# Performance work log

Measured on AMD Instinct MI355X. Metric: run time of the kernel, lower is better.

Reference implementation:

```python
import jax, jax.numpy as jnp
import numpy as np

D_MODEL = 1024
N_HEADS = 16
D_K = D_MODEL // N_HEADS
B, S = 4, 2048


def setup_inputs() -> dict:
    key = jax.random.key(0)
    ks = jax.random.split(key, 9)
    sc = 1.0 / np.sqrt(D_MODEL)
    return {
        "x": jax.random.normal(ks[0], (B, S, D_MODEL), dtype=jnp.float32),
        "Wq": jax.random.normal(ks[1], (D_MODEL, D_MODEL), dtype=jnp.float32) * sc,
        "bq": jax.random.normal(ks[2], (D_MODEL,), dtype=jnp.float32) * 0.02,
        "Wk": jax.random.normal(ks[3], (D_MODEL, D_MODEL), dtype=jnp.float32) * sc,
        "bk": jax.random.normal(ks[4], (D_MODEL,), dtype=jnp.float32) * 0.02,
        "Wv": jax.random.normal(ks[5], (D_MODEL, D_MODEL), dtype=jnp.float32) * sc,
        "bv": jax.random.normal(ks[6], (D_MODEL,), dtype=jnp.float32) * 0.02,
        "Wo": jax.random.normal(ks[7], (D_MODEL, D_MODEL), dtype=jnp.float32) * sc,
        "bo": jax.random.normal(ks[8], (D_MODEL,), dtype=jnp.float32) * 0.02,
    }


def reference(x, Wq, bq, Wk, bk, Wv, bv, Wo, bo):
    b, s, _ = x.shape
    # QKV projections (torch Linear: x @ W.T + b; here weights are stored as [in, out])
    q = (x @ Wq + bq).reshape(b, s, N_HEADS, D_K).transpose(0, 2, 1, 3)  # [b,h,s,dk]
    k = (x @ Wk + bk).reshape(b, s, N_HEADS, D_K).transpose(0, 2, 1, 3)
    v = (x @ Wv + bv).reshape(b, s, N_HEADS, D_K).transpose(0, 2, 1, 3)
    scores = jnp.einsum("bhqd,bhkd->bhqk", q, k) / jnp.sqrt(jnp.float32(D_K))
    attn = jax.nn.softmax(scores, axis=-1)  # dropout=0.0 -> identity
    out = jnp.einsum("bhqk,bhkd->bhqd", attn, v)
    out = out.transpose(0, 2, 1, 3).reshape(b, s, D_MODEL)
    return out @ Wo + bo
```

## Files before the change

### kernel.cpp

```cpp
#include <hip/hip_runtime.h>
#include <hip/hip_bf16.h>

#define DM    1024
#define NH    16
#define DKH   64
#define BB    4
#define SS    2048
#define MROWS (BB*SS)
#define NQK   2048

typedef __attribute__((ext_vector_type(8))) __bf16 bf16x8;
typedef __attribute__((ext_vector_type(4))) float f32x4;
typedef __attribute__((ext_vector_type(16))) float f32x16;
typedef __attribute__((ext_vector_type(4))) unsigned short u16x4;

__device__ __forceinline__ void gload_lds16(const void* g, void* l) {
  __builtin_amdgcn_global_load_lds((const __attribute__((address_space(1))) void*)g,
                                   (__attribute__((address_space(3))) void*)l, 16, 0, 0);
}

__device__ __forceinline__ unsigned short f2bf(float f) {
  __hip_bfloat16 h = __float2bfloat16(f);
  unsigned short u;
  __builtin_memcpy(&u, &h, 2);
  return u;
}

__device__ __forceinline__ unsigned pack2(float a, float b) {
  return (unsigned)f2bf(a) | ((unsigned)f2bf(b) << 16);
}


__global__ __launch_bounds__(256) void cvt_bf16_kernel(const float* __restrict__ in,
                                                       unsigned short* __restrict__ out, int n4) {
  int i = blockIdx.x * 256 + threadIdx.x;
  if (i >= n4) return;
  float4 v = reinterpret_cast<const float4*>(in)[i];
  u16x4 o = { f2bf(v.x), f2bf(v.y), f2bf(v.z), f2bf(v.w) };
  reinterpret_cast<u16x4*>(out)[i] = o;
}

__global__ __launch_bounds__(256) void transpose_cvt_kernel(const float* __restrict__ W,
                                                            unsigned short* __restrict__ WT) {
  __shared__ float t[32][33];
  int tx = threadIdx.x & 31, ty = threadIdx.x >> 5;
  int bx = blockIdx.x * 32, by = blockIdx.y * 32;
#pragma unroll
  for (int i = 0; i < 32; i += 8)
    t[ty + i][tx] = W[(long)(by + ty + i) * DM + bx + tx];
  __syncthreads();
#pragma unroll
  for (int i = 0; i < 32; i += 8)
    WT[(long)(bx + ty + i) * DM + by + tx] = f2bf(t[tx][ty + i]);
}

__global__ void concat2_bias_kernel(const float* __restrict__ a, const float* __restrict__ b,
                                    float* __restrict__ out) {
  int i = blockIdx.x * 256 + threadIdx.x;
  if (i >= NQK) return;
  out[i] = (i < DM) ? a[i] : b[i - DM];
}


__device__ __forceinline__ void store_out(float* p, float v) { *p = v; }
__device__ __forceinline__ void store_out(unsigned short* p, float v) { *p = f2bf(v); }

template <typename OutT, bool Q_SCALE, bool BIAS_ROW>
__global__ __launch_bounds__(256) void gemm_bt_kernel(
    const unsigned short* __restrict__ A,
    const unsigned short* __restrict__ BT,
    const float* __restrict__ bias,
    OutT* __restrict__ C, int M, int N, int K) {
  __shared__ unsigned short As[128 * 32];
  __shared__ unsigned short Bs[128 * 32];
  const int tid = threadIdx.x;
  const int lane = tid & 63;
  const int lr = lane & 15, lg = lane >> 4;
  const int wv = tid >> 6, wm = wv >> 1, wn = wv & 1;
  const long bm = blockIdx.x, bn = blockIdx.y;

  const unsigned short* Ag = A + bm * 128 * K;
  const unsigned short* Bg = BT + bn * 128 * K;

  f32x4 acc[4][4];
#pragma unroll
  for (int i = 0; i < 4; ++i)
#pragma unroll
    for (int j = 0; j < 4; ++j) acc[i][j] = (f32x4){0.f, 0.f, 0.f, 0.f};

  for (int kt = 0; kt < K; kt += 32) {
#pragma unroll
    for (int it = 0; it < 2; ++it) {
      const int e = it * 2048 + tid * 8;
      const int row = e >> 5, col = e & 31;
      gload_lds16(Ag + (long)row * K + kt + col, As + e);
      gload_lds16(Bg + (long)row * K + kt + col, Bs + e);
    }
    __syncthreads();
    bf16x8 af[4], bfr[4];
#pragma unroll
    for (int mi = 0; mi < 4; ++mi)
      af[mi] = *reinterpret_cast<const bf16x8*>(As + (wm * 64 + mi * 16 + lr) * 32 + lg * 8);
#pragma unroll
    for (int ni = 0; ni < 4; ++ni)
      bfr[ni] = *reinterpret_cast<const bf16x8*>(Bs + (wn * 64 + ni * 16 + lr) * 32 + lg * 8);
#pragma unroll
    for (int mi = 0; mi < 4; ++mi)
#pragma unroll
      for (int ni = 0; ni < 4; ++ni)
        acc[mi][ni] = __builtin_amdgcn_mfma_f32_16x16x32_bf16(af[mi], bfr[ni], acc[mi][ni], 0, 0, 0);
    __syncthreads();
  }

#pragma unroll
  for (int ni = 0; ni < 4; ++ni) {
    const int col = (int)bn * 128 + wn * 64 + ni * 16 + lr;
    const float bc = BIAS_ROW ? 0.f : bias[col];
    const float sc = (Q_SCALE && col < DM) ? (0.125f * 1.44269504088896340736f) : 1.0f;
#pragma unroll
    for (int mi = 0; mi < 4; ++mi) {
      const long row0 = bm * 128 + wm * 64 + mi * 16 + lg * 4;
#pragma unroll
      for (int r = 0; r < 4; ++r) {
        const float bv = BIAS_ROW ? bias[row0 + r] : bc;
        float v = (acc[mi][ni][r] + bv) * sc;
        store_out(&C[(row0 + r) * (long)N + col], v);
      }
    }
  }
}


__global__ __launch_bounds__(256, 3) void attn_kernel(
    const unsigned short* __restrict__ QK,
    const unsigned short* __restrict__ Vt,
    unsigned short* __restrict__ AO) {
  __shared__ __align__(16) unsigned char smem[32768];
  unsigned short* K0 = (unsigned short*)smem;
  unsigned short* K1 = (unsigned short*)(smem + 8192);
  unsigned short* V0 = (unsigned short*)(smem + 16384);
  unsigned short* V1 = (unsigned short*)(smem + 24576);

  const int tid = threadIdx.x;
  const int lane = tid & 63;
  const int wv = tid >> 6;
  const int q5 = lane & 31;
  const int hi = lane >> 5;

  const int bh = blockIdx.x;
  const int qt = blockIdx.y;
  const int b = bh >> 4, h = bh & 15;

  const unsigned short* Qp = QK + (long)b * SS * NQK + h * DKH;
  const unsigned short* Kp = Qp + DM;
  const unsigned short* Vp = Vt + (long)h * DKH * MROWS + (long)b * SS;

  bf16x8 qf[4];
  {
    const unsigned short* qrow = Qp + (long)(qt * 128 + wv * 32 + q5) * NQK;
#pragma unroll
    for (int dstep = 0; dstep < 4; ++dstep)
      qf[dstep] = *reinterpret_cast<const bf16x8*>(qrow + dstep * 16 + hi * 8);
  }

  f32x16 accv[2];
#pragma unroll
  for (int d = 0; d < 2; ++d)
#pragma unroll
    for (int r = 0; r < 16; ++r) accv[d][r] = 0.f;
  float m_run = -1e30f, l_run = 0.f;

  f32x16 zc;
#pragma unroll
  for (int r = 0; r < 16; ++r) zc[r] = 0.f;

  f32x16 s4A[2], s4B[2];

  auto stageK = [&](unsigned short* kd, int t) {
#pragma unroll
    for (int it = 0; it < 2; ++it) {
      const int u = it * 256 + tid;
      gload_lds16(Kp + (long)(t * 64 + (u & 63)) * NQK + (u >> 6) * 8, kd + u * 8);
    }
  };
  auto stageV = [&](unsigned short* vd, int t) {
#pragma unroll
    for (int it = 0; it < 2; ++it) {
      const int u = it * 256 + tid;
      gload_lds16(Vp + (long)(u & 63) * MROWS + t * 64 + (u >> 6) * 8, vd + u * 8);
    }
  };

  auto QKf = [&](const unsigned short* K_, f32x16 (&s4)[2]) {
    __builtin_amdgcn_s_setprio(1);
#pragma unroll
    for (int kb = 0; kb < 2; ++kb)
#pragma unroll
      for (int dstep = 0; dstep < 4; ++dstep) {
        bf16x8 kf = *reinterpret_cast<const bf16x8*>(
            K_ + ((dstep * 2 + hi) * 64 + kb * 32 + q5) * 8);
        s4[kb] = __builtin_amdgcn_mfma_f32_32x32x16_bf16(kf, qf[dstep],
                                                         dstep ? s4[kb] : zc, 0, 0, 0);
      }
    __builtin_amdgcn_s_setprio(0);
  };

  auto SMPV = [&](f32x16 (&s4)[2], const unsigned short* V_) {
    float t[16];
#pragma unroll
    for (int r = 0; r < 16; ++r) t[r] = fmaxf(s4[0][r], s4[1][r]);
#pragma unroll
    for (int w = 8; w >= 1; w >>= 1)
#pragma unroll
      for (int r = 0; r < w; ++r) t[r] = fmaxf(t[r], t[r + w]);
    const float mloc = fmaxf(t[0], __shfl_xor(t[0], 32));

    if (!__all(mloc <= m_run + 8.0f)) {
      const float mn = fmaxf(m_run, mloc);
      const float scl = __builtin_amdgcn_exp2f(m_run - mn);
      m_run = mn;
      l_run *= scl;
#pragma unroll
      for (int d = 0; d < 2; ++d)
#pragma unroll
        for (int r = 0; r < 16; ++r) accv[d][r] *= scl;
    }

#pragma unroll
    for (int kb = 0; kb < 2; ++kb)
#pragma unroll
      for (int r = 0; r < 16; ++r)
        s4[kb][r] = __builtin_amdgcn_exp2f(s4[kb][r] - m_run);
    float ts[16];
#pragma unroll
    for (int r = 0; r < 16; ++r) ts[r] = s4[0][r] + s4[1][r];
#pragma unroll
    for (int w = 8; w >= 1; w >>= 1)
#pragma unroll
      for (int r = 0; r < w; ++r) ts[r] += ts[r + w];
    l_run += ts[0] + __shfl_xor(ts[0], 32);

#pragma unroll
    for (int step = 0; step < 4; ++step) {
      const int kb = step >> 1, rb = (step & 1) * 8;
      const unsigned w0 = pack2(s4[kb][rb + 0], s4[kb][rb + 1]);
      const unsigned w1 = pack2(s4[kb][rb + 2], s4[kb][rb + 3]);
      const unsigned w2 = pack2(s4[kb][rb + 4], s4[kb][rb + 5]);
      const unsigned w3 = pack2(s4[kb][rb + 6], s4[kb][rb + 7]);
      const unsigned c = hi ? w0 : w2;
      const unsigned d = hi ? w1 : w3;
      const unsigned xc = (unsigned)__shfl_xor((int)c, 32);
      const unsigned xd = (unsigned)__shfl_xor((int)d, 32);
      union { unsigned u[4]; bf16x8 v; } pf;
      pf.u[0] = hi ? xc : w0;
      pf.u[1] = hi ? xd : w1;
      pf.u[2] = hi ? w2 : xc;
      pf.u[3] = hi ? w3 : xd;
      __builtin_amdgcn_s_setprio(1);
#pragma unroll
      for (int dblk = 0; dblk < 2; ++dblk) {
        bf16x8 vf = *reinterpret_cast<const bf16x8*>(
            V_ + ((step * 2 + hi) * 64 + dblk * 32 + q5) * 8);
        accv[dblk] = __builtin_amdgcn_mfma_f32_32x32x16_bf16(vf, pf.v, accv[dblk], 0, 0, 0);
      }
      __builtin_amdgcn_s_setprio(0);
    }
  };

  stageK(K0, 0);
  __syncthreads();

  stageK(K1, 1);
  stageV(V0, 0);
  QKf(K0, s4A);
  __syncthreads();

#pragma unroll 1
  for (int p = 0; p < 15; ++p) {
    const int i = 1 + 2 * p;
    stageK(K0, i + 1);
    stageV(V1, i);
    QKf(K1, s4B);
    SMPV(s4A, V0);
    __syncthreads();
    stageK(K1, i + 2);
    stageV(V0, i + 1);
    QKf(K0, s4A);
    SMPV(s4B, V1);
    __syncthreads();
  }

  stageV(V1, 31);
  QKf(K1, s4B);
  SMPV(s4A, V0);
  __syncthreads();
  SMPV(s4B, V1);

  const float inv = 1.0f / l_run;
  const long row = (long)b * SS + qt * 128 + wv * 32 + q5;
  unsigned short* orow = AO + row * DM + h * DKH;
#pragma unroll
  for (int dblk = 0; dblk < 2; ++dblk)
#pragma unroll
    for (int j = 0; j < 8; ++j) {
      const int d0 = dblk * 32 + 8 * (j >> 1) + 4 * hi + 2 * (j & 1);
      const unsigned w = pack2(accv[dblk][2 * j] * inv, accv[dblk][2 * j + 1] * inv);
      *reinterpret_cast<unsigned*>(orow + d0) = w;
    }
}


extern "C" void kernel_launch(void* const* d_in, const int* in_sizes, int n_in,
                              void* d_out, int out_size, void* d_ws, size_t ws_size,
                              hipStream_t stream) {
  const float* x  = (const float*)d_in[0];
  const float* Wq = (const float*)d_in[1];
  const float* bq = (const float*)d_in[2];
  const float* Wk = (const float*)d_in[3];
  const float* bk = (const float*)d_in[4];
  const float* Wv = (const float*)d_in[5];
  const float* bv = (const float*)d_in[6];
  const float* Wo = (const float*)d_in[7];
  const float* bo = (const float*)d_in[8];
  float* out = (float*)d_out;

  char* ws = (char*)d_ws;
  size_t off = 0;
  auto alloc = [&](size_t bytes) {
    void* p = ws + off;
    off += (bytes + 255) & ~(size_t)255;
    return p;
  };
  unsigned short* Xb   = (unsigned short*)alloc((size_t)MROWS * DM * 2);
  unsigned short* WTqk = (unsigned short*)alloc((size_t)2 * DM * DM * 2);
  unsigned short* WTv  = (unsigned short*)alloc((size_t)DM * DM * 2);
  unsigned short* WTo  = (unsigned short*)alloc((size_t)DM * DM * 2);
  float*          bqk  = (float*)alloc((size_t)NQK * 4);
  unsigned short* QKb  = (unsigned short*)alloc((size_t)MROWS * NQK * 2);
  unsigned short* Vtb  = (unsigned short*)alloc((size_t)DM * MROWS * 2);
  unsigned short* AOb  = (unsigned short*)alloc((size_t)MROWS * DM * 2);

  cvt_bf16_kernel<<<(MROWS * DM / 4 + 255) / 256, 256, 0, stream>>>(x, Xb, MROWS * DM / 4);
  transpose_cvt_kernel<<<dim3(32, 32), 256, 0, stream>>>(Wq, WTqk);
  transpose_cvt_kernel<<<dim3(32, 32), 256, 0, stream>>>(Wk, WTqk + DM * DM);
  transpose_cvt_kernel<<<dim3(32, 32), 256, 0, stream>>>(Wv, WTv);
  transpose_cvt_kernel<<<dim3(32, 32), 256, 0, stream>>>(Wo, WTo);
  concat2_bias_kernel<<<(NQK + 255) / 256, 256, 0, stream>>>(bq, bk, bqk);

  gemm_bt_kernel<unsigned short, true, false><<<dim3(MROWS / 128, NQK / 128), 256, 0, stream>>>(
      Xb, WTqk, bqk, QKb, MROWS, NQK, DM);
  gemm_bt_kernel<unsigned short, false, true><<<dim3(DM / 128, MROWS / 128), 256, 0, stream>>>(
      WTv, Xb, bv, Vtb, DM, MROWS, DM);

  attn_kernel<<<dim3(BB * NH, SS / 128), 256, 0, stream>>>(QKb, Vtb, AOb);

  gemm_bt_kernel<float, false, false><<<dim3(MROWS / 128, DM / 128), 256, 0, stream>>>(
      AOb, WTo, bo, out, MROWS, DM, DM);
}
```

Baseline: 253.0 us.

## Pre-swizzle K/V into fragment layout and drop LDS staging in attention

After: 255.4 us. About the same (+1.0%).

```diff
diff --git a/kernel.cpp b/kernel.cpp
--- a/kernel.cpp
+++ b/kernel.cpp
@@ -40,8 +40,14 @@
   reinterpret_cast<u16x4*>(out)[i] = o;
 }
 
-__global__ __launch_bounds__(256) void transpose_cvt_kernel(const float* __restrict__ W,
-                                                            unsigned short* __restrict__ WT) {
+__global__ __launch_bounds__(256) void transpose_cvt4_kernel(
+    const float* __restrict__ Wq, const float* __restrict__ Wk,
+    const float* __restrict__ Wv, const float* __restrict__ Wo,
+    unsigned short* __restrict__ WTqk, unsigned short* __restrict__ WTv,
+    unsigned short* __restrict__ WTo) {
+  const int z = blockIdx.z;
+  const float* W = (z == 0) ? Wq : (z == 1) ? Wk : (z == 2) ? Wv : Wo;
+  unsigned short* WT = (z == 0) ? WTqk : (z == 1) ? (WTqk + DM * DM) : (z == 2) ? WTv : WTo;
   __shared__ float t[32][33];
   int tx = threadIdx.x & 31, ty = threadIdx.x >> 5;
   int bx = blockIdx.x * 32, by = blockIdx.y * 32;
@@ -62,15 +68,13 @@
 }
 
 
-__device__ __forceinline__ void store_out(float* p, float v) { *p = v; }
-__device__ __forceinline__ void store_out(unsigned short* p, float v) { *p = f2bf(v); }
-
-template <typename OutT, bool Q_SCALE, bool BIAS_ROW>
+template <int MODE>
 __global__ __launch_bounds__(256) void gemm_bt_kernel(
     const unsigned short* __restrict__ A,
     const unsigned short* __restrict__ BT,
     const float* __restrict__ bias,
-    OutT* __restrict__ C, int M, int N, int K) {
+    void* __restrict__ out0, void* __restrict__ out1,
+    int M, int N, int K) {
   __shared__ unsigned short As[128 * 32];
   __shared__ unsigned short Bs[128 * 32];
   const int tid = threadIdx.x;
@@ -112,19 +116,38 @@
     __syncthreads();
   }
 
+  const float QSC = 0.125f * 1.44269504088896340736f;
 #pragma unroll
   for (int ni = 0; ni < 4; ++ni) {
     const int col = (int)bn * 128 + wn * 64 + ni * 16 + lr;
-    const float bc = BIAS_ROW ? 0.f : bias[col];
-    const float sc = (Q_SCALE && col < DM) ? (0.125f * 1.44269504088896340736f) : 1.0f;
+    const float bc = (MODE == 1) ? 0.f : bias[col];
 #pragma unroll
     for (int mi = 0; mi < 4; ++mi) {
-      const long row0 = bm * 128 + wm * 64 + mi * 16 + lg * 4;
+      const int row0 = (int)bm * 128 + wm * 64 + mi * 16 + lg * 4;
 #pragma unroll
       for (int r = 0; r < 4; ++r) {
-        const float bv = BIAS_ROW ? bias[row0 + r] : bc;
-        float v = (acc[mi][ni][r] + bv) * sc;
-        store_out(&C[(row0 + r) * (long)N + col], v);
+        const int row = row0 + r;
+        float v = acc[mi][ni][r] + ((MODE == 1) ? bias[row] : bc);
+        if (MODE == 0) {
+          if (col < DM) {
+            ((unsigned short*)out0)[(long)row * DM + col] = f2bf(v * QSC);
+          } else {
+            const int c2 = col - DM;
+            const int h = c2 >> 6, dh = c2 & 63;
+            const int b = row >> 11, s = row & 2047;
+            const long idx = ((((long)(b * NH + h) * 32 + (s >> 6)) * 512 +
+                               (dh >> 3) * 64 + (s & 63)) << 3) + (dh & 7);
+            ((unsigned short*)out1)[idx] = f2bf(v);
+          }
+        } else if (MODE == 1) {
+          const int h = row >> 6, dh = row & 63;
+          const int b = col >> 11, s = col & 2047;
+          const long idx = ((((long)(b * NH + h) * 32 + (s >> 6)) * 512 +
+                             ((s >> 3) & 7) * 64 + dh) << 3) + (s & 7);
+          ((unsigned short*)out0)[idx] = f2bf(v);
+        } else {
+          ((float*)out0)[(long)row * N + col] = v;
+        }
       }
     }
   }
@@ -132,15 +155,10 @@
 
 
 __global__ __launch_bounds__(256, 3) void attn_kernel(
-    const unsigned short* __restrict__ QK,
-    const unsigned short* __restrict__ Vt,
+    const unsigned short* __restrict__ Qb,
+    const unsigned short* __restrict__ Kf,
+    const unsigned short* __restrict__ Vf,
     unsigned short* __restrict__ AO) {
-  __shared__ __align__(16) unsigned char smem[32768];
-  unsigned short* K0 = (unsigned short*)smem;
-  unsigned short* K1 = (unsigned short*)(smem + 8192);
-  unsigned short* V0 = (unsigned short*)(smem + 16384);
-  unsigned short* V1 = (unsigned short*)(smem + 24576);
-
   const int tid = threadIdx.x;
   const int lane = tid & 63;
   const int wv = tid >> 6;
@@ -151,18 +169,17 @@
   const int qt = blockIdx.y;
   const int b = bh >> 4, h = bh & 15;
 
-  const unsigned short* Qp = QK + (long)b * SS * NQK + h * DKH;
-  const unsigned short* Kp = Qp + DM;
-  const unsigned short* Vp = Vt + (long)h * DKH * MROWS + (long)b * SS;
-
   bf16x8 qf[4];
   {
-    const unsigned short* qrow = Qp + (long)(qt * 128 + wv * 32 + q5) * NQK;
+    const unsigned short* qrow = Qb + (long)(b * SS + qt * 128 + wv * 32 + q5) * DM + h * DKH;
 #pragma unroll
     for (int dstep = 0; dstep < 4; ++dstep)
       qf[dstep] = *reinterpret_cast<const bf16x8*>(qrow + dstep * 16 + hi * 8);
   }
 
+  const unsigned short* Kp = Kf + (long)bh * 32 * 4096;
+  const unsigned short* Vp = Vf + (long)bh * 32 * 4096;
+
   f32x16 accv[2];
 #pragma unroll
   for (int d = 0; d < 2; ++d)
@@ -174,38 +191,36 @@
 #pragma unroll
   for (int r = 0; r < 16; ++r) zc[r] = 0.f;
 
-  f32x16 s4A[2], s4B[2];
-
-  auto stageK = [&](unsigned short* kd, int t) {
-#pragma unroll
-    for (int it = 0; it < 2; ++it) {
-      const int u = it * 256 + tid;
-      gload_lds16(Kp + (long)(t * 64 + (u & 63)) * NQK + (u >> 6) * 8, kd + u * 8);
-    }
-  };
-  auto stageV = [&](unsigned short* vd, int t) {
-#pragma unroll
-    for (int it = 0; it < 2; ++it) {
-      const int u = it * 256 + tid;
-      gload_lds16(Vp + (long)(u & 63) * MROWS + t * 64 + (u >> 6) * 8, vd + u * 8);
-    }
-  };
-
-  auto QKf = [&](const unsigned short* K_, f32x16 (&s4)[2]) {
+#pragma unroll 1
+  for (int kt = 0; kt < SS / 64; ++kt) {
+    const unsigned short* Kt = Kp + kt * 4096;
+    const unsigned short* Vt = Vp + kt * 4096;
+
+    bf16x8 kf[2][4];
+#pragma unroll
+    for (int kb = 0; kb < 2; ++kb)
+#pragma unroll
+      for (int dstep = 0; dstep < 4; ++dstep)
+        kf[kb][dstep] = *reinterpret_cast<const bf16x8*>(
+            Kt + ((dstep * 2 + hi) * 64 + kb * 32 + q5) * 8);
+    bf16x8 vf[4][2];
+#pragma unroll
+    for (int step = 0; step < 4; ++step)
+#pragma unroll
+      for (int dblk = 0; dblk < 2; ++dblk)
+        vf[step][dblk] = *reinterpret_cast<const bf16x8*>(
+            Vt + ((step * 2 + hi) * 64 + dblk * 32 + q5) * 8);
+
+    f32x16 s4[2];
     __builtin_amdgcn_s_setprio(1);
 #pragma unroll
     for (int kb = 0; kb < 2; ++kb)
 #pragma unroll
-      for (int dstep = 0; dstep < 4; ++dstep) {
-        bf16x8 kf = *reinterpret_cast<const bf16x8*>(
-            K_ + ((dstep * 2 + hi) * 64 + kb * 32 + q5) * 8);
-        s4[kb] = __builtin_amdgcn_mfma_f32_32x32x16_bf16(kf, qf[dstep],
+      for (int dstep = 0; dstep < 4; ++dstep)
+        s4[kb] = __builtin_amdgcn_mfma_f32_32x32x16_bf16(kf[kb][dstep], qf[dstep],
                                                          dstep ? s4[kb] : zc, 0, 0, 0);
-      }
     __builtin_amdgcn_s_setprio(0);
-  };
-
-  auto SMPV = [&](f32x16 (&s4)[2], const unsigned short* V_) {
+
     float t[16];
 #pragma unroll
     for (int r = 0; r < 16; ++r) t[r] = fmaxf(s4[0][r], s4[1][r]);
@@ -258,43 +273,12 @@
       pf.u[3] = hi ? w3 : xd;
       __builtin_amdgcn_s_setprio(1);
 #pragma unroll
-      for (int dblk = 0; dblk < 2; ++dblk) {
-        bf16x8 vf = *reinterpret_cast<const bf16x8*>(
-            V_ + ((step * 2 + hi) * 64 + dblk * 32 + q5) * 8);
-        accv[dblk] = __builtin_amdgcn_mfma_f32_32x32x16_bf16(vf, pf.v, accv[dblk], 0, 0, 0);
-      }
+      for (int dblk = 0; dblk < 2; ++dblk)
+        accv[dblk] = __builtin_amdgcn_mfma_f32_32x32x16_bf16(vf[step][dblk], pf.v,
+                                                             accv[dblk], 0, 0, 0);
       __builtin_amdgcn_s_setprio(0);
     }
-  };
-
-  stageK(K0, 0);
-  __syncthreads();
-
-  stageK(K1, 1);
-  stageV(V0, 0);
-  QKf(K0, s4A);
-  __syncthreads();
-
-#pragma unroll 1
-  for (int p = 0; p < 15; ++p) {
-    const int i = 1 + 2 * p;
-    stageK(K0, i + 1);
-    stageV(V1, i);
-    QKf(K1, s4B);
-    SMPV(s4A, V0);
-    __syncthreads();
-    stageK(K1, i + 2);
-    stageV(V0, i + 1);
-    QKf(K0, s4A);
-    SMPV(s4B, V1);
-    __syncthreads();
   }
-
-  stageV(V1, 31);
-  QKf(K1, s4B);
-  SMPV(s4A, V0);
-  __syncthreads();
-  SMPV(s4B, V1);
 
   const float inv = 1.0f / l_run;
   const long row = (long)b * SS + qt * 128 + wv * 32 + q5;
@@ -336,24 +320,22 @@
   unsigned short* WTv  = (unsigned short*)alloc((size_t)DM * DM * 2);
   unsigned short* WTo  = (unsigned short*)alloc((size_t)DM * DM * 2);
   float*          bqk  = (float*)alloc((size_t)NQK * 4);
-  unsigned short* QKb  = (unsigned short*)alloc((size_t)MROWS * NQK * 2);
-  unsigned short* Vtb  = (unsigned short*)alloc((size_t)DM * MROWS * 2);
+  unsigned short* Qb   = (unsigned short*)alloc((size_t)MROWS * DM * 2);
+  unsigned short* Kb2  = (unsigned short*)alloc((size_t)MROWS * DM * 2);
+  unsigned short* Vb2  = (unsigned short*)alloc((size_t)MROWS * DM * 2);
   unsigned short* AOb  = (unsigned short*)alloc((size_t)MROWS * DM * 2);
 
   cvt_bf16_kernel<<<(MROWS * DM / 4 + 255) / 256, 256, 0, stream>>>(x, Xb, MROWS * DM / 4);
-  transpose_cvt_kernel<<<dim3(32, 32), 256, 0, stream>>>(Wq, WTqk);
-  transpose_cvt_kernel<<<dim3(32, 32), 256, 0, stream>>>(Wk, WTqk + DM * DM);
-  transpose_cvt_kernel<<<dim3(32, 32), 256, 0, stream>>>(Wv, WTv);
-  transpose_cvt_kernel<<<dim3(32, 32), 256, 0, stream>>>(Wo, WTo);
+  transpose_cvt4_kernel<<<dim3(32, 32, 4), 256, 0, stream>>>(Wq, Wk, Wv, Wo, WTqk, WTv, WTo);
   concat2_bias_kernel<<<(NQK + 255) / 256, 256, 0, stream>>>(bq, bk, bqk);
 
-  gemm_bt_kernel<unsigned short, true, false><<<dim3(MROWS / 128, NQK / 128), 256, 0, stream>>>(
-      Xb, WTqk, bqk, QKb, MROWS, NQK, DM);
-  gemm_bt_kernel<unsigned short, false, true><<<dim3(DM / 128, MROWS / 128), 256, 0, stream>>>(
-      WTv, Xb, bv, Vtb, DM, MROWS, DM);
-
-  attn_kernel<<<dim3(BB * NH, SS / 128), 256, 0, stream>>>(QKb, Vtb, AOb);
-
-  gemm_bt_kernel<float, false, false><<<dim3(MROWS / 128, DM / 128), 256, 0, stream>>>(
-      AOb, WTo, bo, out, MROWS, DM, DM);
-}
+  gemm_bt_kernel<0><<<dim3(MROWS / 128, NQK / 128), 256, 0, stream>>>(
+      Xb, WTqk, bqk, Qb, Kb2, MROWS, NQK, DM);
+  gemm_bt_kernel<1><<<dim3(DM / 128, MROWS / 128), 256, 0, stream>>>(
+      WTv, Xb, bv, Vb2, nullptr, DM, MROWS, DM);
+
+  attn_kernel<<<dim3(BB * NH, SS / 128), 256, 0, stream>>>(Qb, Kb2, Vb2, AOb);
+
+  gemm_bt_kernel<2><<<dim3(MROWS / 128, DM / 128), 256, 0, stream>>>(
+      AOb, WTo, bo, out, nullptr, MROWS, DM, DM);
+}
```
